# Kernel optimization log

Hardware: AMD Instinct MI355X
Metric: run time of the kernel (lower is better)

## Reference

```python
import jax, jax.numpy as jnp
import numpy as np

B, N, KD, VD = 2048, 131072, 256, 256

def setup_inputs() -> dict:
    key = jax.random.key(0)
    k1, k2, k3 = jax.random.split(key, 3)
    query = jax.random.normal(k1, (B, KD), dtype=jnp.float32)
    keys = jax.random.normal(k2, (N, KD), dtype=jnp.float32)
    vals = jax.random.normal(k3, (N, VD), dtype=jnp.float32)
    return {"query": query, "keys": keys, "vals": vals, "top_k": 8}

def reference(query, keys, vals, top_k):
    # Pairwise L2 distance via the matmul identity (same math as
    # torch.norm(q[:,None]-k[None], dim=-1), avoids B x N x D intermediate):
    # ||q - k||^2 = ||q||^2 + ||k||^2 - 2 q.k
    q2 = jnp.sum(query * query, axis=-1, keepdims=True)          # [B, 1]
    k2 = jnp.sum(keys * keys, axis=-1)                           # [N]
    qk = jnp.einsum('bd,nd->bn', query, keys)                    # [B, N]
    dist = jnp.sqrt(jnp.maximum(q2 + k2[None, :] - 2.0 * qk, 0.0))
    # top-k smallest distances -> negate and take top-k largest
    _, indices = jax.lax.top_k(-dist, top_k)                     # [B, k]
    retrieved = vals[indices]                                    # [B, k, VD]
    return retrieved
```

## Files before the change

kernel.cpp:

```cpp
#include <hip/hip_runtime.h>
#include <hip/hip_bf16.h>
#include <cstdint>

#define B_Q    2048
#define N_K    131072
#define KD     256
#define VD     256
#define TOPK   8

#define TK     32
#define NCHUNK 64
#define CHUNK  (N_K / NCHUNK)
#define CTILES (CHUNK / TK)
#define QB     256
#define QTILES (B_Q / QB)
#define QBS    256
#define NBUF   4
#define TILE_B (TK * KD * 2)
#define SSTEPS 8
#define SLOTS  32
#define OVCAP  8192
#define NSUB   16
#define TAU_MARGIN 2.0f
#define SENTF  0x7F800000u

typedef short bf16x8 __attribute__((ext_vector_type(8)));
typedef float f32x4  __attribute__((ext_vector_type(4)));

__device__ __forceinline__ unsigned short f2bf(float x) {
    uint32_t u = __float_as_uint(x);
    uint32_t r = (u + 0x7FFFu + ((u >> 16) & 1u)) >> 16;
    return (unsigned short)r;
}

__device__ __forceinline__ bool lex_lt(float d1, int i1, float d2, int i2) {
    return (d1 < d2) || (d1 == d2 && i1 < i2);
}

__device__ __forceinline__ uint32_t umin32(uint32_t a, uint32_t b) { return a < b ? a : b; }
__device__ __forceinline__ uint32_t umax32(uint32_t a, uint32_t b) { return a > b ? a : b; }
__device__ __forceinline__ unsigned long long umin64(unsigned long long a, unsigned long long b) { return a < b ? a : b; }

__device__ __forceinline__ void gld16(const void* g, void* l) {
    __builtin_amdgcn_global_load_lds(
        (const __attribute__((address_space(1))) unsigned int*)g,
        (__attribute__((address_space(3))) unsigned int*)l, 16, 0, 0);
}
__device__ __forceinline__ void gld4(const void* g, void* l) {
    __builtin_amdgcn_global_load_lds(
        (const __attribute__((address_space(1))) unsigned int*)g,
        (__attribute__((address_space(3))) unsigned int*)l, 4, 0, 0);
}

__device__ __forceinline__ void ins8u(uint32_t v, uint32_t (&c)[8]) {
    if (v < c[7]) {
        c[7] = v;
        #pragma unroll
        for (int p = 7; p > 0; --p)
            if (c[p] < c[p - 1]) { uint32_t t = c[p]; c[p] = c[p - 1]; c[p - 1] = t; }
    }
}

__global__ void qprep_kernel(const float* __restrict__ q, float* __restrict__ q2,
                             unsigned short* __restrict__ qa) {
    int gw   = (blockIdx.x * blockDim.x + threadIdx.x) >> 6;
    int lane = threadIdx.x & 63;
    float4 v = reinterpret_cast<const float4*>(q + (size_t)gw * KD)[lane];
    float s = v.x * v.x + v.y * v.y + v.z * v.z + v.w * v.w;
    #pragma unroll
    for (int off = 32; off > 0; off >>= 1) s += __shfl_down(s, off, 64);
    if (lane == 0) q2[gw] = s;
    ushort4 u;
    u.x = f2bf(-2.f * v.x); u.y = f2bf(-2.f * v.y);
    u.z = f2bf(-2.f * v.z); u.w = f2bf(-2.f * v.w);
    *reinterpret_cast<ushort4*>(qa + (size_t)gw * KD + lane * 4) = u;
}

__global__ __launch_bounds__(256) void kperm2_kernel(
    const float* __restrict__ keys, unsigned short* __restrict__ kp,
    float* __restrict__ k2) {
    __shared__ float psum[32][33];
    const int gt = blockIdx.x, tid = threadIdx.x;
    #pragma unroll
    for (int u = 0; u < 4; ++u) {
        int unit = u * 256 + tid;
        int row  = unit >> 5;
        int grp  = unit & 31;
        const float* src = keys + (size_t)(gt * 32 + row) * KD + grp * 8;
        float4 a = *reinterpret_cast<const float4*>(src);
        float4 b = *reinterpret_cast<const float4*>(src + 4);
        psum[row][grp] = a.x * a.x + a.y * a.y + a.z * a.z + a.w * a.w
                       + b.x * b.x + b.y * b.y + b.z * b.z + b.w * b.w;
        uint4 pack;
        pack.x = (uint32_t)f2bf(a.x) | ((uint32_t)f2bf(a.y) << 16);
        pack.y = (uint32_t)f2bf(a.z) | ((uint32_t)f2bf(a.w) << 16);
        pack.z = (uint32_t)f2bf(b.x) | ((uint32_t)f2bf(b.y) << 16);
        pack.w = (uint32_t)f2bf(b.z) | ((uint32_t)f2bf(b.w) << 16);
        int s  = grp >> 2;
        int ki = row >> 4;
        int l  = ((grp & 3) << 4) | (row & 15);
        size_t o = ((((size_t)gt * 8 + s) * 2 + ki) * 64 + l);
        *reinterpret_cast<uint4*>(kp + o * 8) = pack;
    }
    __syncthreads();
    if (tid < 32) {
        float s = 0.f;
        #pragma unroll
        for (int g = 0; g < 32; ++g) s += psum[tid][g];
        k2[gt * 32 + tid] = s;
    }
}

__global__ __launch_bounds__(512, 2) void sample_kernel(
    const unsigned short* __restrict__ qaug, const char* __restrict__ kperm,
    const float* __restrict__ k2, uint32_t* __restrict__ subtop) {

    __shared__ __align__(16) char  lds[TILE_B];
    __shared__ __align__(16) float k2l[64];

    const int tid = threadIdx.x;
    const int w   = tid >> 6;
    const int l   = tid & 63;
    const int l15 = l & 15;
    const int l4  = l >> 4;
    const int sub = blockIdx.x & (NSUB - 1);
    const int qt  = blockIdx.x >> 4;
    const int q0  = qt * QBS;

    bf16x8 af[2][SSTEPS];
    #pragma unroll
    for (int qf = 0; qf < 2; ++qf)
        #pragma unroll
        for (int s = 0; s < SSTEPS; ++s) {
            int qr = q0 + w * 32 + qf * 16 + l15;
            af[qf][s] = *reinterpret_cast<const bf16x8*>(
                qaug + (size_t)qr * KD + s * 32 + l4 * 8);
        }

    uint32_t cnd[2][4][8];
    #pragma unroll
    for (int qf = 0; qf < 2; ++qf)
        #pragma unroll
        for (int j = 0; j < 4; ++j)
            #pragma unroll
            for (int s = 0; s < 8; ++s) cnd[qf][j][s] = SENTF;

    for (int i = 0; i < 4; ++i) {
        int t = sub * 4 + i;
        __syncthreads();
        const char* src = kperm + (size_t)t * TILE_B;
        #pragma unroll
        for (int i2 = 0; i2 < 2; ++i2) {
            int seg = w * 2 + i2;
            gld16(src + seg * 1024 + l * 16, &lds[seg * 1024]);
        }
        gld4(k2 + t * TK + l, &k2l[0]);
        __syncthreads();

        float k2v[2];
        #pragma unroll
        for (int ki = 0; ki < 2; ++ki) k2v[ki] = k2l[ki * 16 + l15] + 256.0f;

        f32x4 acc[2][2];
        #pragma unroll
        for (int qf = 0; qf < 2; ++qf)
            #pragma unroll
            for (int ki = 0; ki < 2; ++ki) acc[qf][ki] = (f32x4){0.f, 0.f, 0.f, 0.f};

        #pragma unroll
        for (int s = 0; s < SSTEPS; ++s) {
            bf16x8 bfr[2];
            #pragma unroll
            for (int ki = 0; ki < 2; ++ki)
                bfr[ki] = *reinterpret_cast<const bf16x8*>(&lds[((s * 2 + ki) * 64 + l) * 16]);
            #pragma unroll
            for (int ki = 0; ki < 2; ++ki) {
                acc[0][ki] = __builtin_amdgcn_mfma_f32_16x16x32_bf16(af[0][s], bfr[ki], acc[0][ki], 0, 0, 0);
                acc[1][ki] = __builtin_amdgcn_mfma_f32_16x16x32_bf16(af[1][s], bfr[ki], acc[1][ki], 0, 0, 0);
            }
        }

        #pragma unroll
        for (int qf = 0; qf < 2; ++qf)
            #pragma unroll
            for (int j = 0; j < 4; ++j) {
                ins8u(__float_as_uint(k2v[0] + acc[qf][0][j]), cnd[qf][j]);
                ins8u(__float_as_uint(k2v[1] + acc[qf][1][j]), cnd[qf][j]);
            }
    }

    #pragma unroll
    for (int qf = 0; qf < 2; ++qf)
        #pragma unroll
        for (int j = 0; j < 4; ++j) {
            uint32_t c[8];
            #pragma unroll
            for (int s = 0; s < 8; ++s) c[s] = cnd[qf][j][s];
            #pragma unroll
            for (int mask = 1; mask <= 8; mask <<= 1) {
                uint32_t o[8], m[8];
                #pragma unroll
                for (int s = 0; s < 8; ++s)
                    o[s] = (uint32_t)__shfl_xor((int)c[s], mask, 64);
                #pragma unroll
                for (int s = 0; s < 8; ++s) m[s] = umin32(c[s], o[7 - s]);
                #define CX(a,b) { uint32_t lo = umin32(m[a], m[b]); uint32_t hi = umax32(m[a], m[b]); m[a] = lo; m[b] = hi; }
                CX(0,4) CX(1,5) CX(2,6) CX(3,7)
                CX(0,2) CX(1,3) CX(4,6) CX(5,7)
                CX(0,1) CX(2,3) CX(4,5) CX(6,7)
                #undef CX
                #pragma unroll
                for (int s = 0; s < 8; ++s) c[s] = m[s];
            }
            if (l15 == 0) {
                int q = q0 + w * 32 + qf * 16 + l4 * 4 + j;
                uint32_t* dst = subtop + ((size_t)q * NSUB + sub) * 8;
                uint4 a = {c[0], c[1], c[2], c[3]};
                uint4 b = {c[4], c[5], c[6], c[7]};
                *reinterpret_cast<uint4*>(dst)     = a;
                *reinterpret_cast<uint4*>(dst + 4) = b;
            }
        }
}

__global__ void tau_kernel(const uint32_t* __restrict__ subtop, float* __restrict__ taug,
                           uint32_t* __restrict__ ovcnt) {
    int q = blockIdx.x * 256 + threadIdx.x;
    uint32_t c[8];
    #pragma unroll
    for (int s = 0; s < 8; ++s) c[s] = SENTF;
    for (int i = 0; i < NSUB * 8; ++i) ins8u(subtop[(size_t)q * NSUB * 8 + i], c);
    taug[q] = __uint_as_float(c[7]) + TAU_MARGIN;
    if (q == 0) *ovcnt = 0;
}

__global__ __launch_bounds__(512, 4) void phase1_kernel(
    const unsigned short* __restrict__ qaug, const char* __restrict__ kperm,
    const float* __restrict__ k2, const float* __restrict__ taug,
    uint32_t* __restrict__ list, uint32_t* __restrict__ cnt2,
    uint32_t* __restrict__ ovcnt, unsigned long long* __restrict__ ovlist) {

    __shared__ __align__(16) char     lds[NBUF][TILE_B];
    __shared__ __align__(16) float    k2l[NBUF][64];
    __shared__            uint32_t    scnt[QB];

    const int tid   = threadIdx.x;
    const int w     = tid >> 6;
    const int l     = tid & 63;
    const int l15   = l & 15;
    const int l4    = l >> 4;
    const int chunk = blockIdx.x & (NCHUNK - 1);
    const int qt    = blockIdx.x >> 6;
    const int q0    = qt * QB;
    const char*  kpb = kperm + (size_t)chunk * ((size_t)CTILES * TILE_B);
    const float* k2c = k2 + (size_t)chunk * CHUNK;

    if (tid < QB) scnt[tid] = 0;

    bf16x8 af[2][SSTEPS];
    float  tau[2][4];
    #pragma unroll
    for (int qf = 0; qf < 2; ++qf) {
        #pragma unroll
        for (int s = 0; s < SSTEPS; ++s) {
            int qr = q0 + w * 32 + qf * 16 + l15;
            af[qf][s] = *reinterpret_cast<const bf16x8*>(
                qaug + (size_t)qr * KD + s * 32 + l4 * 8);
        }
        #pragma unroll
        for (int j = 0; j < 4; ++j)
            tau[qf][j] = taug[q0 + w * 32 + qf * 16 + l4 * 4 + j];
    }

    auto STAGE = [&](int t) {
        int buf = t & (NBUF - 1);
        const char* src = kpb + (size_t)t * TILE_B;
        #pragma unroll
        for (int i = 0; i < 2; ++i) {
            int seg = w * 2 + i;
            gld16(src + seg * 1024 + l * 16, &lds[buf][seg * 1024]);
        }
        gld4(k2c + t * TK + l, &k2l[buf][0]);
    };

    STAGE(0); STAGE(1); STAGE(2);

    for (int t = 0; t < CTILES; ++t) {
        const int buf = t & (NBUF - 1);
        if (t < CTILES - 2)       asm volatile("s_waitcnt vmcnt(6)" ::: "memory");
        else if (t == CTILES - 2) asm volatile("s_waitcnt vmcnt(3)" ::: "memory");
        else                      asm volatile("s_waitcnt vmcnt(0)" ::: "memory");
        __builtin_amdgcn_s_barrier();
        __builtin_amdgcn_sched_barrier(0);

        const char* lb = &lds[buf][0];
        float k2v[2];
        #pragma unroll
        for (int ki = 0; ki < 2; ++ki) k2v[ki] = k2l[buf][ki * 16 + l15] + 256.0f;

        f32x4 acc[2][2];
        #pragma unroll
        for (int qf = 0; qf < 2; ++qf)
            #pragma unroll
            for (int ki = 0; ki < 2; ++ki) acc[qf][ki] = (f32x4){0.f, 0.f, 0.f, 0.f};

        #pragma unroll
        for (int s = 0; s < SSTEPS; ++s) {
            bf16x8 bfr[2];
            #pragma unroll
            for (int ki = 0; ki < 2; ++ki)
                bfr[ki] = *reinterpret_cast<const bf16x8*>(lb + ((s * 2 + ki) * 64 + l) * 16);
            #pragma unroll
            for (int ki = 0; ki < 2; ++ki) {
                acc[0][ki] = __builtin_amdgcn_mfma_f32_16x16x32_bf16(af[0][s], bfr[ki], acc[0][ki], 0, 0, 0);
                acc[1][ki] = __builtin_amdgcn_mfma_f32_16x16x32_bf16(af[1][s], bfr[ki], acc[1][ki], 0, 0, 0);
            }
        }

        const uint32_t kb = (uint32_t)(t * TK + l15);
        #pragma unroll
        for (int qf = 0; qf < 2; ++qf)
            #pragma unroll
            for (int j = 0; j < 4; ++j) {
                float v0 = k2v[0] + acc[qf][0][j];
                float v1 = k2v[1] + acc[qf][1][j];
                float tq = tau[qf][j];
                int   ql = w * 32 + qf * 16 + l4 * 4 + j;
                if (v0 < tq) {
                    uint32_t slot = atomicAdd(&scnt[ql], 1u);
                    uint32_t e = (__float_as_uint(v0) & 0xFFFFF800u) | kb;
                    if (slot < SLOTS) {
                        list[(((size_t)(q0 + ql) * NCHUNK + chunk) << 5) + slot] = e;
                    } else {
                        uint32_t op = atomicAdd(ovcnt, 1u);
                        if (op < OVCAP)
                            ovlist[op] = ((unsigned long long)__float_as_uint(v0) << 32)
                                       | ((unsigned long long)(uint32_t)(q0 + ql) << 17)
                                       | (uint32_t)(chunk * CHUNK + kb);
                    }
                }
                if (v1 < tq) {
                    uint32_t slot = atomicAdd(&scnt[ql], 1u);
                    uint32_t e = (__float_as_uint(v1) & 0xFFFFF800u) | (kb + 16u);
                    if (slot < SLOTS) {
                        list[(((size_t)(q0 + ql) * NCHUNK + chunk) << 5) + slot] = e;
                    } else {
                        uint32_t op = atomicAdd(ovcnt, 1u);
                        if (op < OVCAP)
                            ovlist[op] = ((unsigned long long)__float_as_uint(v1) << 32)
                                       | ((unsigned long long)(uint32_t)(q0 + ql) << 17)
                                       | (uint32_t)(chunk * CHUNK + kb + 16u);
                    }
                }
            }

        if (t + 3 < CTILES) STAGE(t + 3);
    }

    __syncthreads();
    if (tid < QB) cnt2[(size_t)(q0 + tid) * NCHUNK + chunk] = umin32(scnt[tid], SLOTS);
}

__global__ __launch_bounds__(256) void phase2_kernel(
    const uint32_t* __restrict__ list, const uint32_t* __restrict__ cnt2,
    const uint32_t* __restrict__ ovcnt, const unsigned long long* __restrict__ ovlist,
    const float* __restrict__ query, const float* __restrict__ keys,
    const float* __restrict__ q2g, const float* __restrict__ k2g,
    const float* __restrict__ vals, float* __restrict__ out) {

    __shared__ uint32_t cc[NCHUNK];
    __shared__ unsigned long long ovq[64];
    __shared__ uint32_t nov;
    __shared__ int topg[64];
    __shared__ float td2[64];
    __shared__ int fin[8];

    const int q = blockIdx.x, tid = threadIdx.x, w = tid >> 6, l = tid & 63;

    if (tid < NCHUNK) cc[tid] = cnt2[(size_t)q * NCHUNK + tid];
    if (tid < 64) ovq[tid] = ~0ull;
    if (tid == 0) nov = 0;
    __syncthreads();
    uint32_t on = umin32(*ovcnt, OVCAP);
    for (uint32_t i = tid; i < on; i += 256) {
        unsigned long long e = ovlist[i];
        if (((e >> 17) & 0x7FFull) == (unsigned long long)q) {
            uint32_t p = atomicAdd(&nov, 1u);
            if (p < 64)
                ovq[p] = ((unsigned long long)((uint32_t)(e >> 32) >> 11) << 17)
                       | (uint32_t)(e & 0x1FFFFull);
        }
    }
    __syncthreads();

    unsigned long long v[9];
    #pragma unroll
    for (int j = 0; j < 9; ++j) {
        int idx = j * 64 + l;
        unsigned long long key = ~0ull;
        if (idx < 512) {
            int c = w * 16 + (idx >> 5), s = idx & 31;
            if ((uint32_t)s < cc[c]) {
                uint32_t e = list[(((size_t)q * NCHUNK + c) << 5) + s];
                key = ((unsigned long long)(e >> 11) << 17)
                    | (uint32_t)(c * CHUNK + (e & 0x7FFu));
            }
        } else if (idx < 528) {
            key = ovq[w * 16 + (idx - 512)];
        }
        v[j] = key;
    }

    for (int r = 0; r < 16; ++r) {
        unsigned long long bv = v[0];
        #pragma unroll
        for (int j = 1; j < 9; ++j) bv = umin64(bv, v[j]);
        #pragma unroll
        for (int off = 32; off > 0; off >>= 1) {
            unsigned long long ov = __shfl_xor(bv, off, 64);
            bv = umin64(bv, ov);
        }
        if (l == 0) topg[w * 16 + r] = (bv == ~0ull) ? -1 : (int)(uint32_t)(bv & 0x1FFFFull);
        #pragma unroll
        for (int j = 0; j < 9; ++j) if (v[j] == bv) v[j] = ~0ull;
    }
    __syncthreads();

    float4 qv = reinterpret_cast<const float4*>(query + (size_t)q * KD)[l];
    for (int r = w; r < 64; r += 4) {
        int gk = topg[r];
        if (gk >= 0) {
            float4 kv = reinterpret_cast<const float4*>(keys + (size_t)gk * KD)[l];
            float d = qv.x * kv.x + qv.y * kv.y + qv.z * kv.z + qv.w * kv.w;
            #pragma unroll
            for (int off = 32; off > 0; off >>= 1) d += __shfl_down(d, off, 64);
            if (l == 0) td2[r] = fmaxf(q2g[q] + k2g[gk] - 2.0f * d, 0.0f);
        } else if (l == 0) {
            td2[r] = INFINITY;
        }
    }
    __syncthreads();

    if (tid == 0) {
        float fd[8]; int fi[8];
        #pragma unroll
        for (int s = 0; s < 8; ++s) { fd[s] = INFINITY; fi[s] = 0x7fffffff; }
        for (int i = 0; i < 64; ++i) {
            if (topg[i] < 0) continue;
            float d2 = td2[i]; int gk = topg[i];
            if (lex_lt(d2, gk, fd[7], fi[7])) {
                fd[7] = d2; fi[7] = gk;
                #pragma unroll
                for (int p = 7; p > 0; --p)
                    if (lex_lt(fd[p], fi[p], fd[p - 1], fi[p - 1])) {
                        float t1 = fd[p]; fd[p] = fd[p - 1]; fd[p - 1] = t1;
                        int   t2 = fi[p]; fi[p] = fi[p - 1]; fi[p - 1] = t2;
                    }
            }
        }
        #pragma unroll
        for (int s = 0; s < 8; ++s) fin[s] = fi[s];
    }
    __syncthreads();

    for (int r = w; r < TOPK; r += 4) {
        float4 v2 = reinterpret_cast<const float4*>(vals + (size_t)fin[r] * VD)[l];
        reinterpret_cast<float4*>(out + ((size_t)q * TOPK + r) * VD)[l] = v2;
    }
}

extern "C" void kernel_launch(void* const* d_in, const int* in_sizes, int n_in,
                              void* d_out, int out_size, void* d_ws, size_t ws_size,
                              hipStream_t stream) {
    const float* query = (const float*)d_in[0];
    const float* keys  = (const float*)d_in[1];
    const float* vals  = (const float*)d_in[2];
    float* out = (float*)d_out;

    char* ws = (char*)d_ws;
    float*              q2     = (float*)(ws);
    float*              k2     = (float*)(ws + 8192);
    unsigned short*     qaug   = (unsigned short*)(ws + 533504);
    unsigned short*     kperm  = (unsigned short*)(ws + 1582080);
    uint32_t*           list   = (uint32_t*)(ws + 68690944);
    uint32_t*           subtop = (uint32_t*)(ws + 68690944);
    uint32_t*           cnt2   = (uint32_t*)(ws + 85468160);
    float*              taug   = (float*)(ws + 85992448);
    uint32_t*           ovcnt  = (uint32_t*)(ws + 86000640);
    unsigned long long* ovlist = (unsigned long long*)(ws + 86004736);

    qprep_kernel<<<B_Q / 4, 256, 0, stream>>>(query, q2, qaug);
    kperm2_kernel<<<N_K / 32, 256, 0, stream>>>(keys, kperm, k2);
    sample_kernel<<<(B_Q / QBS) * NSUB, 512, 0, stream>>>(qaug, (const char*)kperm, k2, subtop);
    tau_kernel<<<B_Q / 256, 256, 0, stream>>>(subtop, taug, ovcnt);
    phase1_kernel<<<NCHUNK * QTILES, 512, 0, stream>>>(qaug, (const char*)kperm, k2,
                                                       taug, list, cnt2, ovcnt, ovlist);
    phase2_kernel<<<B_Q, 256, 0, stream>>>(list, cnt2, ovcnt, ovlist,
                                           query, keys, q2, k2, vals, out);
}
```

Before: 324.4 us.

## Parallelize tau reduction across wavefronts and double phase1 block to 16 waves

The tau kernel now gives each query a full wavefront, which merges the 128 subtop candidates with xor-shuffle bitonic merges instead of one thread doing serial insertion. Phase1 moves from 8 waves handling 32 queries each to 16 waves handling 16 queries each, so each wave issues half the MFMAs and one staging load per tile. This aims to spread the same block's work over more waves to hide latency, at the cost of twice the LDS B-fragment reads per useful MFMA and a 1024-thread block that may limit occupancy.

```diff
diff --git a/kernel.cpp b/kernel.cpp
--- a/kernel.cpp
+++ b/kernel.cpp
@@ -223,18 +223,38 @@
         }
 }
 
-__global__ void tau_kernel(const uint32_t* __restrict__ subtop, float* __restrict__ taug,
-                           uint32_t* __restrict__ ovcnt) {
-    int q = blockIdx.x * 256 + threadIdx.x;
+__global__ __launch_bounds__(256) void tau_kernel(
+    const uint32_t* __restrict__ subtop, float* __restrict__ taug,
+    uint32_t* __restrict__ ovcnt) {
+    const int tid = threadIdx.x, l = tid & 63;
+    const int q = blockIdx.x * 4 + (tid >> 6);
+    uint32_t a = subtop[(size_t)q * 128 + l];
+    uint32_t b = subtop[(size_t)q * 128 + 64 + l];
     uint32_t c[8];
-    #pragma unroll
-    for (int s = 0; s < 8; ++s) c[s] = SENTF;
-    for (int i = 0; i < NSUB * 8; ++i) ins8u(subtop[(size_t)q * NSUB * 8 + i], c);
-    taug[q] = __uint_as_float(c[7]) + TAU_MARGIN;
-    if (q == 0) *ovcnt = 0;
-}
-
-__global__ __launch_bounds__(512, 4) void phase1_kernel(
+    c[0] = umin32(a, b); c[1] = umax32(a, b);
+    #pragma unroll
+    for (int s = 2; s < 8; ++s) c[s] = SENTF;
+    #pragma unroll
+    for (int mask = 1; mask <= 32; mask <<= 1) {
+        uint32_t o[8], m[8];
+        #pragma unroll
+        for (int s = 0; s < 8; ++s)
+            o[s] = (uint32_t)__shfl_xor((int)c[s], mask, 64);
+        #pragma unroll
+        for (int s = 0; s < 8; ++s) m[s] = umin32(c[s], o[7 - s]);
+        #define CX(x,y) { uint32_t lo = umin32(m[x], m[y]); uint32_t hi = umax32(m[x], m[y]); m[x] = lo; m[y] = hi; }
+        CX(0,4) CX(1,5) CX(2,6) CX(3,7)
+        CX(0,2) CX(1,3) CX(4,6) CX(5,7)
+        CX(0,1) CX(2,3) CX(4,5) CX(6,7)
+        #undef CX
+        #pragma unroll
+        for (int s = 0; s < 8; ++s) c[s] = m[s];
+    }
+    if (l == 0) taug[q] = __uint_as_float(c[7]) + TAU_MARGIN;
+    if (blockIdx.x == 0 && tid == 0) *ovcnt = 0;
+}
+
+__global__ __launch_bounds__(1024, 4) void phase1_kernel(
     const unsigned short* __restrict__ qaug, const char* __restrict__ kperm,
     const float* __restrict__ k2, const float* __restrict__ taug,
     uint32_t* __restrict__ list, uint32_t* __restrict__ cnt2,
@@ -257,29 +277,22 @@
 
     if (tid < QB) scnt[tid] = 0;
 
-    bf16x8 af[2][SSTEPS];
-    float  tau[2][4];
-    #pragma unroll
-    for (int qf = 0; qf < 2; ++qf) {
-        #pragma unroll
-        for (int s = 0; s < SSTEPS; ++s) {
-            int qr = q0 + w * 32 + qf * 16 + l15;
-            af[qf][s] = *reinterpret_cast<const bf16x8*>(
-                qaug + (size_t)qr * KD + s * 32 + l4 * 8);
-        }
-        #pragma unroll
-        for (int j = 0; j < 4; ++j)
-            tau[qf][j] = taug[q0 + w * 32 + qf * 16 + l4 * 4 + j];
-    }
+    bf16x8 af[SSTEPS];
+    float  tau[4];
+    #pragma unroll
+    for (int s = 0; s < SSTEPS; ++s) {
+        int qr = q0 + w * 16 + l15;
+        af[s] = *reinterpret_cast<const bf16x8*>(
+            qaug + (size_t)qr * KD + s * 32 + l4 * 8);
+    }
+    #pragma unroll
+    for (int j = 0; j < 4; ++j)
+        tau[j] = taug[q0 + w * 16 + l4 * 4 + j];
 
     auto STAGE = [&](int t) {
         int buf = t & (NBUF - 1);
         const char* src = kpb + (size_t)t * TILE_B;
-        #pragma unroll
-        for (int i = 0; i < 2; ++i) {
-            int seg = w * 2 + i;
-            gld16(src + seg * 1024 + l * 16, &lds[buf][seg * 1024]);
-        }
+        gld16(src + w * 1024 + l * 16, &lds[buf][w * 1024]);
         gld4(k2c + t * TK + l, &k2l[buf][0]);
     };
 
@@ -287,8 +300,8 @@
 
     for (int t = 0; t < CTILES; ++t) {
         const int buf = t & (NBUF - 1);
-        if (t < CTILES - 2)       asm volatile("s_waitcnt vmcnt(6)" ::: "memory");
-        else if (t == CTILES - 2) asm volatile("s_waitcnt vmcnt(3)" ::: "memory");
+        if (t < CTILES - 2)       asm volatile("s_waitcnt vmcnt(4)" ::: "memory");
+        else if (t == CTILES - 2) asm volatile("s_waitcnt vmcnt(2)" ::: "memory");
         else                      asm volatile("s_waitcnt vmcnt(0)" ::: "memory");
         __builtin_amdgcn_s_barrier();
         __builtin_amdgcn_sched_barrier(0);
@@ -298,11 +311,9 @@
         #pragma unroll
         for (int ki = 0; ki < 2; ++ki) k2v[ki] = k2l[buf][ki * 16 + l15] + 256.0f;
 
-        f32x4 acc[2][2];
-        #pragma unroll
-        for (int qf = 0; qf < 2; ++qf)
-            #pragma unroll
-            for (int ki = 0; ki < 2; ++ki) acc[qf][ki] = (f32x4){0.f, 0.f, 0.f, 0.f};
+        f32x4 acc[2];
+        #pragma unroll
+        for (int ki = 0; ki < 2; ++ki) acc[ki] = (f32x4){0.f, 0.f, 0.f, 0.f};
 
         #pragma unroll
         for (int s = 0; s < SSTEPS; ++s) {
@@ -311,48 +322,44 @@
             for (int ki = 0; ki < 2; ++ki)
                 bfr[ki] = *reinterpret_cast<const bf16x8*>(lb + ((s * 2 + ki) * 64 + l) * 16);
             #pragma unroll
-            for (int ki = 0; ki < 2; ++ki) {
-                acc[0][ki] = __builtin_amdgcn_mfma_f32_16x16x32_bf16(af[0][s], bfr[ki], acc[0][ki], 0, 0, 0);
-                acc[1][ki] = __builtin_amdgcn_mfma_f32_16x16x32_bf16(af[1][s], bfr[ki], acc[1][ki], 0, 0, 0);
-            }
+            for (int ki = 0; ki < 2; ++ki)
+                acc[ki] = __builtin_amdgcn_mfma_f32_16x16x32_bf16(af[s], bfr[ki], acc[ki], 0, 0, 0);
         }
 
         const uint32_t kb = (uint32_t)(t * TK + l15);
         #pragma unroll
-        for (int qf = 0; qf < 2; ++qf)
-            #pragma unroll
-            for (int j = 0; j < 4; ++j) {
-                float v0 = k2v[0] + acc[qf][0][j];
-                float v1 = k2v[1] + acc[qf][1][j];
-                float tq = tau[qf][j];
-                int   ql = w * 32 + qf * 16 + l4 * 4 + j;
-                if (v0 < tq) {
-                    uint32_t slot = atomicAdd(&scnt[ql], 1u);
-                    uint32_t e = (__float_as_uint(v0) & 0xFFFFF800u) | kb;
-                    if (slot < SLOTS) {
-                        list[(((size_t)(q0 + ql) * NCHUNK + chunk) << 5) + slot] = e;
-                    } else {
-                        uint32_t op = atomicAdd(ovcnt, 1u);
-                        if (op < OVCAP)
-                            ovlist[op] = ((unsigned long long)__float_as_uint(v0) << 32)
-                                       | ((unsigned long long)(uint32_t)(q0 + ql) << 17)
-                                       | (uint32_t)(chunk * CHUNK + kb);
-                    }
+        for (int j = 0; j < 4; ++j) {
+            float v0 = k2v[0] + acc[0][j];
+            float v1 = k2v[1] + acc[1][j];
+            float tq = tau[j];
+            int   ql = w * 16 + l4 * 4 + j;
+            if (v0 < tq) {
+                uint32_t slot = atomicAdd(&scnt[ql], 1u);
+                uint32_t e = (__float_as_uint(v0) & 0xFFFFF800u) | kb;
+                if (slot < SLOTS) {
+                    list[(((size_t)(q0 + ql) * NCHUNK + chunk) << 5) + slot] = e;
+                } else {
+                    uint32_t op = atomicAdd(ovcnt, 1u);
+                    if (op < OVCAP)
+                        ovlist[op] = ((unsigned long long)__float_as_uint(v0) << 32)
+                                   | ((unsigned long long)(uint32_t)(q0 + ql) << 17)
+                                   | (uint32_t)(chunk * CHUNK + kb);
                 }
-                if (v1 < tq) {
-                    uint32_t slot = atomicAdd(&scnt[ql], 1u);
-                    uint32_t e = (__float_as_uint(v1) & 0xFFFFF800u) | (kb + 16u);
-                    if (slot < SLOTS) {
-                        list[(((size_t)(q0 + ql) * NCHUNK + chunk) << 5) + slot] = e;
-                    } else {
-                        uint32_t op = atomicAdd(ovcnt, 1u);
-                        if (op < OVCAP)
-                            ovlist[op] = ((unsigned long long)__float_as_uint(v1) << 32)
-                                       | ((unsigned long long)(uint32_t)(q0 + ql) << 17)
-                                       | (uint32_t)(chunk * CHUNK + kb + 16u);
-                    }
+            }
+            if (v1 < tq) {
+                uint32_t slot = atomicAdd(&scnt[ql], 1u);
+                uint32_t e = (__float_as_uint(v1) & 0xFFFFF800u) | (kb + 16u);
+                if (slot < SLOTS) {
+                    list[(((size_t)(q0 + ql) * NCHUNK + chunk) << 5) + slot] = e;
+                } else {
+                    uint32_t op = atomicAdd(ovcnt, 1u);
+                    if (op < OVCAP)
+                        ovlist[op] = ((unsigned long long)__float_as_uint(v1) << 32)
+                                   | ((unsigned long long)(uint32_t)(q0 + ql) << 17)
+                                   | (uint32_t)(chunk * CHUNK + kb + 16u);
                 }
             }
+        }
 
         if (t + 3 < CTILES) STAGE(t + 3);
     }
@@ -492,9 +499,9 @@
     qprep_kernel<<<B_Q / 4, 256, 0, stream>>>(query, q2, qaug);
     kperm2_kernel<<<N_K / 32, 256, 0, stream>>>(keys, kperm, k2);
     sample_kernel<<<(B_Q / QBS) * NSUB, 512, 0, stream>>>(qaug, (const char*)kperm, k2, subtop);
-    tau_kernel<<<B_Q / 256, 256, 0, stream>>>(subtop, taug, ovcnt);
-    phase1_kernel<<<NCHUNK * QTILES, 512, 0, stream>>>(qaug, (const char*)kperm, k2,
-                                                       taug, list, cnt2, ovcnt, ovlist);
+    tau_kernel<<<B_Q / 4, 256, 0, stream>>>(subtop, taug, ovcnt);
+    phase1_kernel<<<NCHUNK * QTILES, 1024, 0, stream>>>(qaug, (const char*)kperm, k2,
+                                                        taug, list, cnt2, ovcnt, ovlist);
     phase2_kernel<<<B_Q, 256, 0, stream>>>(list, cnt2, ovcnt, ovlist,
                                            query, keys, q2, k2, vals, out);
 }
```

Result: faster. 280.8 us (-13.5%).
